# Kernel tuning notes

Measured on AMD Instinct MI355X. Metric: run time of the kernel, lower is better.

Reference implementation:

```python
import jax, jax.numpy as jnp
import numpy as np

N, K, D = 500000, 16, 16


def setup_inputs() -> dict:
    key = jax.random.key(0)
    k1, k2, k3, k4 = jax.random.split(key, 4)
    x = jax.random.normal(k1, (N, D), dtype=jnp.float32)
    # mixture weights: positive, sum to 1, shape (1, K)
    pi = jax.nn.softmax(jax.random.normal(k2, (1, K), dtype=jnp.float32), axis=-1)
    mu = jax.random.normal(k3, (K, 1, D), dtype=jnp.float32)
    # SPD covariance per cluster: A A^T / D + I
    A = jax.random.normal(k4, (K, D, D), dtype=jnp.float32)
    Sigma = jnp.einsum('kde,kfe->kdf', A, A) / D + jnp.eye(D, dtype=jnp.float32)
    return {"x": x, "pi": pi, "mu": mu, "Sigma": Sigma}


def reference(x, pi, mu, Sigma):
    # Batched MultivariateNormal log_prob over K clusters (replaces the
    # Python loop over torch.distributions.MultivariateNormal).
    d = x.shape[-1]
    L = jnp.linalg.cholesky(Sigma)                      # (K, D, D)
    diff = x[None, :, :] - mu                           # (K, N, D) via mu (K,1,D)
    # solve L y = diff^T per cluster -> Mahalanobis = ||y||^2
    y = jax.vmap(lambda Lk, dk: jax.scipy.linalg.solve_triangular(Lk, dk.T, lower=True))(L, diff)  # (K, D, N)
    maha = jnp.sum(y * y, axis=1)                       # (K, N)
    half_logdet = jnp.sum(jnp.log(jnp.diagonal(L, axis1=-2, axis2=-1)), axis=-1)  # (K,)
    log2pi = jnp.log(jnp.asarray(2.0 * np.pi, dtype=x.dtype))
    logp = -0.5 * (maha + d * log2pi) - half_logdet[:, None]  # (K, N)
    res_k = jnp.exp(logp).T * pi                        # (N, K), pi broadcasts from (1,K)
    res = res_k / jnp.sum(res_k, axis=1, keepdims=True)  # (N, K)
    return res
```

## Files before the change

kernel.cpp:

```cpp
#include <hip/hip_runtime.h>
#include <math.h>

#define D 16
#define K 16
#define BLK 256
#define PK_WORDS 96

typedef _Float16 h2 __attribute__((ext_vector_type(2)));

__host__ __device__ constexpr int tri(int i, int j) { return i * (i + 1) / 2 + j; }
__host__ __device__ constexpr int rowoff(int i) {
    int s = 0;
    for (int r = 0; r < i; ++r) s += (r + 2) / 2;
    return s;
}

static __device__ __forceinline__ float fdot2f(h2 a, h2 b, float c) {
#if __has_builtin(__builtin_amdgcn_fdot2)
    return __builtin_amdgcn_fdot2(a, b, c, false);
#else
    return fmaf((float)a.x, (float)b.x, fmaf((float)a.y, (float)b.y, c));
#endif
}

static __device__ __forceinline__ unsigned pack2(float f0, float f1) {
    _Float16 h0 = (_Float16)f0, h1 = (_Float16)f1;
    unsigned short b0 = __builtin_bit_cast(unsigned short, h0);
    unsigned short b1 = __builtin_bit_cast(unsigned short, h1);
    return ((unsigned)b1 << 16) | (unsigned)b0;
}

__global__ __launch_bounds__(64) void gmm_prep(
    const float* __restrict__ pi, const float* __restrict__ mu,
    const float* __restrict__ Sigma, float* __restrict__ P)
{
    const int k = threadIdx.x;
    if (k >= K) return;

    float M[tri(D - 1, D - 1) + 1];

#pragma unroll
    for (int i = 0; i < D; ++i)
#pragma unroll
        for (int j = 0; j <= i; ++j)
            M[tri(i, j)] = Sigma[k * D * D + i * D + j];

    float hl = 0.f;
#pragma unroll
    for (int j = 0; j < D; ++j) {
        float s = M[tri(j, j)];
#pragma unroll
        for (int p = 0; p < j; ++p) s -= M[tri(j, p)] * M[tri(j, p)];
        float ljj = sqrtf(s);
        M[tri(j, j)] = ljj;
        hl += logf(ljj);
        float inv = 1.f / ljj;
#pragma unroll
        for (int i = j + 1; i < D; ++i) {
            float t = M[tri(i, j)];
#pragma unroll
            for (int p = 0; p < j; ++p) t -= M[tri(i, p)] * M[tri(j, p)];
            M[tri(i, j)] = t * inv;
        }
    }

#pragma unroll
    for (int j = 0; j < D; ++j) {
        float ujj = 1.f / M[tri(j, j)];
        M[tri(j, j)] = ujj;
#pragma unroll
        for (int i = j + 1; i < D; ++i) {
            float s = 0.f;
#pragma unroll
            for (int p = j; p < i; ++p) s += M[tri(i, p)] * M[tri(p, j)];
            M[tri(i, j)] = -s / M[tri(i, i)];
        }
    }

    const float invs2 = 0.70710678118654752440f;
    float* Pk = P + k * PK_WORDS;
    unsigned* Pu = (unsigned*)Pk;

    Pk[0] = logf(pi[k]) - hl;
#pragma unroll
    for (int i = 0; i < D; ++i) {
        float acc = 0.f;
#pragma unroll
        for (int j = 0; j <= i; ++j) acc += M[tri(i, j)] * mu[k * D + j];
        Pk[1 + i] = -(acc * invs2);
    }
#pragma unroll
    for (int i = 0; i < D; ++i) {
        const int np = (i + 2) / 2;
#pragma unroll
        for (int p = 0; p < np; ++p) {
            float f0 = M[tri(i, 2 * p)] * invs2;
            float f1 = (2 * p + 1 <= i) ? M[tri(i, 2 * p + 1)] * invs2 : 0.f;
            Pu[17 + rowoff(i) + p] = pack2(f0, f1);
        }
    }
#pragma unroll
    for (int q = 89; q < PK_WORDS; ++q) Pu[q] = 0;
}

__global__ __launch_bounds__(BLK) void gmm_main(
    const float* __restrict__ x, const float* __restrict__ P,
    float* __restrict__ out, int N)
{
    const int tid = threadIdx.x;
    const long long n = (long long)blockIdx.x * BLK + tid;
    const bool ok = n < (long long)N;

    float4 xr0 = {0, 0, 0, 0}, xr1 = xr0, xr2 = xr0, xr3 = xr0;
    if (ok) {
        const float4* p = (const float4*)(x + n * D);
        xr0 = p[0]; xr1 = p[1]; xr2 = p[2]; xr3 = p[3];
    }

    h2 xp[8];
    xp[0] = (h2){(_Float16)xr0.x, (_Float16)xr0.y};
    xp[1] = (h2){(_Float16)xr0.z, (_Float16)xr0.w};
    xp[2] = (h2){(_Float16)xr1.x, (_Float16)xr1.y};
    xp[3] = (h2){(_Float16)xr1.z, (_Float16)xr1.w};
    xp[4] = (h2){(_Float16)xr2.x, (_Float16)xr2.y};
    xp[5] = (h2){(_Float16)xr2.z, (_Float16)xr2.w};
    xp[6] = (h2){(_Float16)xr3.x, (_Float16)xr3.y};
    xp[7] = (h2){(_Float16)xr3.z, (_Float16)xr3.w};

    float r[K];
#pragma unroll
    for (int k = 0; k < K; ++k) {
        const float* __restrict__ Pk = P + k * PK_WORDS;
        const unsigned* __restrict__ Uk = (const unsigned*)(Pk + 17);
        float acc = 0.f;
#pragma unroll
        for (int i = 0; i < D; ++i) {
            float y = Pk[1 + i];
            const int np = (i + 2) / 2;
#pragma unroll
            for (int p = 0; p < np; ++p) {
                h2 u = __builtin_bit_cast(h2, Uk[rowoff(i) + p]);
                y = fdot2f(u, xp[p], y);
            }
            acc = fmaf(y, y, acc);
        }
        r[k] = Pk[0] - acc;
    }

    float mx = r[0];
#pragma unroll
    for (int k = 1; k < K; ++k) mx = fmaxf(mx, r[k]);
    float sum = 0.f;
#pragma unroll
    for (int k = 0; k < K; ++k) {
        float e = __expf(r[k] - mx);
        r[k] = e;
        sum += e;
    }
    float inv = 1.f / sum;
    if (ok) {
        float4* po = (float4*)(out + n * D);
        po[0] = (float4){r[0] * inv,  r[1] * inv,  r[2] * inv,  r[3] * inv};
        po[1] = (float4){r[4] * inv,  r[5] * inv,  r[6] * inv,  r[7] * inv};
        po[2] = (float4){r[8] * inv,  r[9] * inv,  r[10] * inv, r[11] * inv};
        po[3] = (float4){r[12] * inv, r[13] * inv, r[14] * inv, r[15] * inv};
    }
}

extern "C" void kernel_launch(void* const* d_in, const int* in_sizes, int n_in,
                              void* d_out, int out_size, void* d_ws, size_t ws_size,
                              hipStream_t stream) {
    const float* x     = (const float*)d_in[0];
    const float* pi    = (const float*)d_in[1];
    const float* mu    = (const float*)d_in[2];
    const float* Sigma = (const float*)d_in[3];
    float* out = (float*)d_out;
    const int N = in_sizes[0] / D;

    float* P = (float*)d_ws;

    gmm_prep<<<1, 64, 0, stream>>>(pi, mu, Sigma, P);

    const int grid = (N + BLK - 1) / BLK;
    gmm_main<<<grid, BLK, 0, stream>>>(x, P, out, N);
}
```

Before: 118.6 us.

## Map clusters to lanes with register-resident factors and persistent prefetching grid

Each lane now handles one cluster for one of four points per wavefront, keeping that cluster's packed inverse-Cholesky factors and offsets in registers instead of reloading all sixteen clusters' parameters per point. The softmax over clusters becomes a 16-lane shuffle reduction. A fixed 1024-block grid-stride loop prefetches the next point's row while computing the current one. Each lane redundantly loads the full 64-byte x row, and outputs become scalar stores, which may cost bandwidth efficiency.

```diff
diff --git a/kernel.cpp b/kernel.cpp
--- a/kernel.cpp
+++ b/kernel.cpp
@@ -4,6 +4,7 @@
 #define D 16
 #define K 16
 #define BLK 256
+#define GRID 1024
 #define PK_WORDS 96
 
 typedef _Float16 h2 __attribute__((ext_vector_type(2)));
@@ -103,67 +104,92 @@
     for (int q = 89; q < PK_WORDS; ++q) Pu[q] = 0;
 }
 
-__global__ __launch_bounds__(BLK) void gmm_main(
+__global__ __launch_bounds__(BLK, 3) void gmm_main(
     const float* __restrict__ x, const float* __restrict__ P,
     float* __restrict__ out, int N)
 {
-    const int tid = threadIdx.x;
-    const long long n = (long long)blockIdx.x * BLK + tid;
-    const bool ok = n < (long long)N;
-
-    float4 xr0 = {0, 0, 0, 0}, xr1 = xr0, xr2 = xr0, xr3 = xr0;
-    if (ok) {
+    const int tid  = threadIdx.x;
+    const int lane = tid & 63;
+    const int k    = lane & 15;
+    const int q    = lane >> 4;
+
+    const long long wid = (long long)blockIdx.x * (BLK / 64) + (tid >> 6);
+    const long long nw  = (long long)gridDim.x * (BLK / 64);
+    const long long G   = ((long long)N + 3) >> 2;
+
+    const float* __restrict__ Pk = P + k * PK_WORDS;
+    const unsigned* __restrict__ Uk = (const unsigned*)(Pk + 17);
+    const float ck = Pk[0];
+    float nt[D];
+#pragma unroll
+    for (int i = 0; i < D; ++i) nt[i] = Pk[1 + i];
+    unsigned Ur[72];
+#pragma unroll
+    for (int p = 0; p < 72; ++p) Ur[p] = Uk[p];
+
+    if (wid >= G) return;
+
+    long long g = wid;
+    float4 xa0, xa1, xa2, xa3;
+    {
+        long long n = g * 4 + q;
+        if (n >= N) n = N - 1;
         const float4* p = (const float4*)(x + n * D);
-        xr0 = p[0]; xr1 = p[1]; xr2 = p[2]; xr3 = p[3];
-    }
-
-    h2 xp[8];
-    xp[0] = (h2){(_Float16)xr0.x, (_Float16)xr0.y};
-    xp[1] = (h2){(_Float16)xr0.z, (_Float16)xr0.w};
-    xp[2] = (h2){(_Float16)xr1.x, (_Float16)xr1.y};
-    xp[3] = (h2){(_Float16)xr1.z, (_Float16)xr1.w};
-    xp[4] = (h2){(_Float16)xr2.x, (_Float16)xr2.y};
-    xp[5] = (h2){(_Float16)xr2.z, (_Float16)xr2.w};
-    xp[6] = (h2){(_Float16)xr3.x, (_Float16)xr3.y};
-    xp[7] = (h2){(_Float16)xr3.z, (_Float16)xr3.w};
-
-    float r[K];
-#pragma unroll
-    for (int k = 0; k < K; ++k) {
-        const float* __restrict__ Pk = P + k * PK_WORDS;
-        const unsigned* __restrict__ Uk = (const unsigned*)(Pk + 17);
+        xa0 = p[0]; xa1 = p[1]; xa2 = p[2]; xa3 = p[3];
+    }
+
+    while (true) {
+        const long long g_next = g + nw;
+
+        float4 xb0, xb1, xb2, xb3;
+        {
+            long long n = g_next * 4 + q;
+            if (g_next >= G || n >= N) n = 0;
+            const float4* p = (const float4*)(x + n * D);
+            xb0 = p[0]; xb1 = p[1]; xb2 = p[2]; xb3 = p[3];
+        }
+
+        h2 xp[8];
+        xp[0] = (h2){(_Float16)xa0.x, (_Float16)xa0.y};
+        xp[1] = (h2){(_Float16)xa0.z, (_Float16)xa0.w};
+        xp[2] = (h2){(_Float16)xa1.x, (_Float16)xa1.y};
+        xp[3] = (h2){(_Float16)xa1.z, (_Float16)xa1.w};
+        xp[4] = (h2){(_Float16)xa2.x, (_Float16)xa2.y};
+        xp[5] = (h2){(_Float16)xa2.z, (_Float16)xa2.w};
+        xp[6] = (h2){(_Float16)xa3.x, (_Float16)xa3.y};
+        xp[7] = (h2){(_Float16)xa3.z, (_Float16)xa3.w};
+
         float acc = 0.f;
 #pragma unroll
         for (int i = 0; i < D; ++i) {
-            float y = Pk[1 + i];
+            float y = nt[i];
             const int np = (i + 2) / 2;
 #pragma unroll
-            for (int p = 0; p < np; ++p) {
-                h2 u = __builtin_bit_cast(h2, Uk[rowoff(i) + p]);
-                y = fdot2f(u, xp[p], y);
-            }
+            for (int p = 0; p < np; ++p)
+                y = fdot2f(__builtin_bit_cast(h2, Ur[rowoff(i) + p]), xp[p], y);
             acc = fmaf(y, y, acc);
         }
-        r[k] = Pk[0] - acc;
-    }
-
-    float mx = r[0];
-#pragma unroll
-    for (int k = 1; k < K; ++k) mx = fmaxf(mx, r[k]);
-    float sum = 0.f;
-#pragma unroll
-    for (int k = 0; k < K; ++k) {
-        float e = __expf(r[k] - mx);
-        r[k] = e;
-        sum += e;
-    }
-    float inv = 1.f / sum;
-    if (ok) {
-        float4* po = (float4*)(out + n * D);
-        po[0] = (float4){r[0] * inv,  r[1] * inv,  r[2] * inv,  r[3] * inv};
-        po[1] = (float4){r[4] * inv,  r[5] * inv,  r[6] * inv,  r[7] * inv};
-        po[2] = (float4){r[8] * inv,  r[9] * inv,  r[10] * inv, r[11] * inv};
-        po[3] = (float4){r[12] * inv, r[13] * inv, r[14] * inv, r[15] * inv};
+        const float logit = ck - acc;
+
+        float m = logit;
+        m = fmaxf(m, __shfl_xor(m, 1));
+        m = fmaxf(m, __shfl_xor(m, 2));
+        m = fmaxf(m, __shfl_xor(m, 4));
+        m = fmaxf(m, __shfl_xor(m, 8));
+        const float e = __expf(logit - m);
+        float s = e;
+        s += __shfl_xor(s, 1);
+        s += __shfl_xor(s, 2);
+        s += __shfl_xor(s, 4);
+        s += __shfl_xor(s, 8);
+
+        const long long n = g * 4 + q;
+        if (n < (long long)N)
+            out[n * K + k] = e / s;
+
+        if (g_next >= G) break;
+        g = g_next;
+        xa0 = xb0; xa1 = xb1; xa2 = xb2; xa3 = xb3;
     }
 }
 
@@ -181,6 +207,5 @@
 
     gmm_prep<<<1, 64, 0, stream>>>(pi, mu, Sigma, P);
 
-    const int grid = (N + BLK - 1) / BLK;
-    gmm_main<<<grid, BLK, 0, stream>>>(x, P, out, N);
-}
+    gmm_main<<<GRID, BLK, 0, stream>>>(x, P, out, N);
+}
```

After: 139.5 us. +17.6%, slower.

## Recast Mahalanobis as quadratic-feature matmul on MFMA with persistent grid

Applied to the files above, without the earlier changes.

Expands each cluster's quadratic form into weights over pairwise products x_i*x_j plus linear and constant terms, precomputed in the prep kernel. The main kernel builds fp16 product features per row and evaluates all 16 clusters with 16x16x32 f16 MFMA instructions. The softmax over clusters is done with cross-lane shuffles. A fixed persistent grid with next-tile prefetch of x replaces one thread per row. The aim is to move the triangular-solve dot products onto matrix cores, at the cost of fp16 rounding on products of x, which may hurt accuracy for large |x|.

```diff
diff --git a/kernel.cpp b/kernel.cpp
--- a/kernel.cpp
+++ b/kernel.cpp
@@ -4,41 +4,32 @@
 #define D 16
 #define K 16
 #define BLK 256
-#define PK_WORDS 96
-
-typedef _Float16 h2 __attribute__((ext_vector_type(2)));
+#define GRID 1024
+#define NFEAT 160
+
+typedef __fp16 f16x8 __attribute__((ext_vector_type(8)));
+typedef float  f32x4 __attribute__((ext_vector_type(4)));
 
 __host__ __device__ constexpr int tri(int i, int j) { return i * (i + 1) / 2 + j; }
-__host__ __device__ constexpr int rowoff(int i) {
-    int s = 0;
-    for (int r = 0; r < i; ++r) s += (r + 2) / 2;
-    return s;
-}
-
-static __device__ __forceinline__ float fdot2f(h2 a, h2 b, float c) {
-#if __has_builtin(__builtin_amdgcn_fdot2)
-    return __builtin_amdgcn_fdot2(a, b, c, false);
-#else
-    return fmaf((float)a.x, (float)b.x, fmaf((float)a.y, (float)b.y, c));
-#endif
-}
-
-static __device__ __forceinline__ unsigned pack2(float f0, float f1) {
-    _Float16 h0 = (_Float16)f0, h1 = (_Float16)f1;
-    unsigned short b0 = __builtin_bit_cast(unsigned short, h0);
-    unsigned short b1 = __builtin_bit_cast(unsigned short, h1);
-    return ((unsigned)b1 << 16) | (unsigned)b0;
+
+static __device__ __forceinline__ unsigned short f16b(float f) {
+    _Float16 h = (_Float16)f;
+    return __builtin_bit_cast(unsigned short, h);
+}
+static __device__ __forceinline__ unsigned pkrtz(float a, float b) {
+    auto t = __builtin_amdgcn_cvt_pkrtz(a, b);
+    return __builtin_bit_cast(unsigned, t);
 }
 
 __global__ __launch_bounds__(64) void gmm_prep(
     const float* __restrict__ pi, const float* __restrict__ mu,
-    const float* __restrict__ Sigma, float* __restrict__ P)
+    const float* __restrict__ Sigma, unsigned short* __restrict__ W,
+    float* __restrict__ cvals)
 {
     const int k = threadIdx.x;
     if (k >= K) return;
 
-    float M[tri(D - 1, D - 1) + 1];
-
+    float M[136];
 #pragma unroll
     for (int i = 0; i < D; ++i)
 #pragma unroll
@@ -63,7 +54,6 @@
             M[tri(i, j)] = t * inv;
         }
     }
-
 #pragma unroll
     for (int j = 0; j < D; ++j) {
         float ujj = 1.f / M[tri(j, j)];
@@ -76,94 +66,138 @@
             M[tri(i, j)] = -s / M[tri(i, i)];
         }
     }
-
     const float invs2 = 0.70710678118654752440f;
-    float* Pk = P + k * PK_WORDS;
-    unsigned* Pu = (unsigned*)Pk;
-
-    Pk[0] = logf(pi[k]) - hl;
+#pragma unroll
+    for (int t = 0; t < 136; ++t) M[t] *= invs2;
+
+    float tv[D];
+    float gamma = 0.f;
 #pragma unroll
     for (int i = 0; i < D; ++i) {
-        float acc = 0.f;
-#pragma unroll
-        for (int j = 0; j <= i; ++j) acc += M[tri(i, j)] * mu[k * D + j];
-        Pk[1 + i] = -(acc * invs2);
-    }
-#pragma unroll
-    for (int i = 0; i < D; ++i) {
-        const int np = (i + 2) / 2;
-#pragma unroll
-        for (int p = 0; p < np; ++p) {
-            float f0 = M[tri(i, 2 * p)] * invs2;
-            float f1 = (2 * p + 1 <= i) ? M[tri(i, 2 * p + 1)] * invs2 : 0.f;
-            Pu[17 + rowoff(i) + p] = pack2(f0, f1);
-        }
-    }
-#pragma unroll
-    for (int q = 89; q < PK_WORDS; ++q) Pu[q] = 0;
-}
-
-__global__ __launch_bounds__(BLK) void gmm_main(
-    const float* __restrict__ x, const float* __restrict__ P,
-    float* __restrict__ out, int N)
+        float a = 0.f;
+#pragma unroll
+        for (int j = 0; j <= i; ++j) a += M[tri(i, j)] * mu[k * D + j];
+        tv[i] = a;
+        gamma += a * a;
+    }
+    cvals[k] = logf(pi[k]) - hl - gamma;
+
+    unsigned short* Wk = W + k * NFEAT;
+#pragma unroll
+    for (int d = 0; d <= 8; ++d)
+#pragma unroll
+        for (int i = 0; i < D; ++i) {
+            const int b = (i + d) & 15;
+            const int lo = (i < b) ? i : b;
+            const int hi = (i < b) ? b : i;
+            float s = 0.f;
+#pragma unroll
+            for (int t = hi; t < D; ++t) s += M[tri(t, lo)] * M[tri(t, hi)];
+            const float w = (d == 0) ? -s : ((d == 8) ? -s : -2.f * s);
+            Wk[16 * d + i] = f16b(w);
+        }
+#pragma unroll
+    for (int m = 0; m < D; ++m) {
+        float s = 0.f;
+#pragma unroll
+        for (int t = m; t < D; ++t) s += tv[t] * M[tri(t, m)];
+        Wk[144 + m] = f16b(2.f * s);
+    }
+}
+
+__global__ __launch_bounds__(BLK, 4) void gmm_main(
+    const float* __restrict__ x, const unsigned short* __restrict__ W,
+    const float* __restrict__ cvals, float* __restrict__ out, int N)
 {
-    const int tid = threadIdx.x;
-    const long long n = (long long)blockIdx.x * BLK + tid;
-    const bool ok = n < (long long)N;
-
-    float4 xr0 = {0, 0, 0, 0}, xr1 = xr0, xr2 = xr0, xr3 = xr0;
-    if (ok) {
-        const float4* p = (const float4*)(x + n * D);
-        xr0 = p[0]; xr1 = p[1]; xr2 = p[2]; xr3 = p[3];
-    }
-
-    h2 xp[8];
-    xp[0] = (h2){(_Float16)xr0.x, (_Float16)xr0.y};
-    xp[1] = (h2){(_Float16)xr0.z, (_Float16)xr0.w};
-    xp[2] = (h2){(_Float16)xr1.x, (_Float16)xr1.y};
-    xp[3] = (h2){(_Float16)xr1.z, (_Float16)xr1.w};
-    xp[4] = (h2){(_Float16)xr2.x, (_Float16)xr2.y};
-    xp[5] = (h2){(_Float16)xr2.z, (_Float16)xr2.w};
-    xp[6] = (h2){(_Float16)xr3.x, (_Float16)xr3.y};
-    xp[7] = (h2){(_Float16)xr3.z, (_Float16)xr3.w};
-
-    float r[K];
-#pragma unroll
-    for (int k = 0; k < K; ++k) {
-        const float* __restrict__ Pk = P + k * PK_WORDS;
-        const unsigned* __restrict__ Uk = (const unsigned*)(Pk + 17);
-        float acc = 0.f;
-#pragma unroll
-        for (int i = 0; i < D; ++i) {
-            float y = Pk[1 + i];
-            const int np = (i + 2) / 2;
-#pragma unroll
-            for (int p = 0; p < np; ++p) {
-                h2 u = __builtin_bit_cast(h2, Uk[rowoff(i) + p]);
-                y = fdot2f(u, xp[p], y);
+    const int tid  = threadIdx.x;
+    const int lane = tid & 63;
+    const int col  = lane & 15;
+    const int quad = lane >> 4;
+    const bool qhi = (quad & 2) != 0;
+    const int i0   = (quad & 1) * 8;
+
+    f16x8 Af[5];
+#pragma unroll
+    for (int s = 0; s < 5; ++s) {
+        const uint4* p = (const uint4*)(W + col * NFEAT + s * 32 + quad * 8);
+        uint4 v = *p;
+        Af[s] = __builtin_bit_cast(f16x8, v);
+    }
+    const f32x4 cv = *(const f32x4*)(cvals + quad * 4);
+
+    const long long T  = ((long long)N + 15) >> 4;
+    long long tile     = (long long)blockIdx.x * (BLK / 64) + (tid >> 6);
+    const long long nw = (long long)GRID * (BLK / 64);
+    if (tile >= T) return;
+
+    float4 xa0, xa1, xa2, xa3;
+    {
+        long long n = tile * 16 + col;
+        if (n >= N) n = N - 1;
+        const float* row = x + n * D;
+        xa0 = *(const float4*)(row + i0);
+        xa1 = *(const float4*)(row + i0 + 4);
+        xa2 = *(const float4*)(row + (i0 ^ 8));
+        xa3 = *(const float4*)(row + (i0 ^ 8) + 4);
+    }
+
+    while (true) {
+        const long long tnext = tile + nw;
+        float4 xb0, xb1, xb2, xb3;
+        {
+            long long n2 = tnext * 16 + col;
+            if (tnext >= T || n2 >= (long long)N) n2 = 0;
+            const float* row = x + n2 * D;
+            xb0 = *(const float4*)(row + i0);
+            xb1 = *(const float4*)(row + i0 + 4);
+            xb2 = *(const float4*)(row + (i0 ^ 8));
+            xb3 = *(const float4*)(row + (i0 ^ 8) + 4);
+        }
+
+        const float xr[16] = {xa0.x, xa0.y, xa0.z, xa0.w,
+                              xa1.x, xa1.y, xa1.z, xa1.w,
+                              xa2.x, xa2.y, xa2.z, xa2.w,
+                              xa3.x, xa3.y, xa3.z, xa3.w};
+
+        f32x4 acc = {0.f, 0.f, 0.f, 0.f};
+#pragma unroll
+        for (int s = 0; s < 5; ++s) {
+            float pr[8];
+#pragma unroll
+            for (int j = 0; j < 8; ++j) {
+                float xbv;
+                if (s < 4)
+                    xbv = qhi ? xr[(j + 2 * s + 1) & 15] : xr[(j + 2 * s) & 15];
+                else
+                    xbv = qhi ? 1.0f : xr[(j + 8) & 15];
+                pr[j] = xr[j] * xbv;
             }
-            acc = fmaf(y, y, acc);
-        }
-        r[k] = Pk[0] - acc;
-    }
-
-    float mx = r[0];
-#pragma unroll
-    for (int k = 1; k < K; ++k) mx = fmaxf(mx, r[k]);
-    float sum = 0.f;
-#pragma unroll
-    for (int k = 0; k < K; ++k) {
-        float e = __expf(r[k] - mx);
-        r[k] = e;
-        sum += e;
-    }
-    float inv = 1.f / sum;
-    if (ok) {
-        float4* po = (float4*)(out + n * D);
-        po[0] = (float4){r[0] * inv,  r[1] * inv,  r[2] * inv,  r[3] * inv};
-        po[1] = (float4){r[4] * inv,  r[5] * inv,  r[6] * inv,  r[7] * inv};
-        po[2] = (float4){r[8] * inv,  r[9] * inv,  r[10] * inv, r[11] * inv};
-        po[3] = (float4){r[12] * inv, r[13] * inv, r[14] * inv, r[15] * inv};
+            uint4 bw = {pkrtz(pr[0], pr[1]), pkrtz(pr[2], pr[3]),
+                        pkrtz(pr[4], pr[5]), pkrtz(pr[6], pr[7])};
+            f16x8 Bf = __builtin_bit_cast(f16x8, bw);
+            acc = __builtin_amdgcn_mfma_f32_16x16x32_f16(Af[s], Bf, acc, 0, 0, 0);
+        }
+
+        f32x4 l = acc + cv;
+        float mx = fmaxf(fmaxf(l.x, l.y), fmaxf(l.z, l.w));
+        mx = fmaxf(mx, __shfl_xor(mx, 16));
+        mx = fmaxf(mx, __shfl_xor(mx, 32));
+        float e0 = __expf(l.x - mx), e1 = __expf(l.y - mx);
+        float e2 = __expf(l.z - mx), e3 = __expf(l.w - mx);
+        float ss = e0 + e1 + e2 + e3;
+        ss += __shfl_xor(ss, 16);
+        ss += __shfl_xor(ss, 32);
+        const float inv = 1.f / ss;
+
+        const long long n = tile * 16 + col;
+        if (n < (long long)N) {
+            float4* po = (float4*)(out + n * K + quad * 4);
+            *po = (float4){e0 * inv, e1 * inv, e2 * inv, e3 * inv};
+        }
+
+        if (tnext >= T) break;
+        tile = tnext;
+        xa0 = xb0; xa1 = xb1; xa2 = xb2; xa3 = xb3;
     }
 }
 
@@ -177,10 +211,9 @@
     float* out = (float*)d_out;
     const int N = in_sizes[0] / D;
 
-    float* P = (float*)d_ws;
-
-    gmm_prep<<<1, 64, 0, stream>>>(pi, mu, Sigma, P);
-
-    const int grid = (N + BLK - 1) / BLK;
-    gmm_main<<<grid, BLK, 0, stream>>>(x, P, out, N);
-}
+    unsigned short* W = (unsigned short*)d_ws;
+    float* cvals = (float*)((char*)d_ws + K * NFEAT * sizeof(unsigned short));
+
+    gmm_prep<<<1, 64, 0, stream>>>(pi, mu, Sigma, W, cvals);
+    gmm_main<<<GRID, BLK, 0, stream>>>(x, W, cvals, out, N);
+}
```

Result: slower. 131.1 us (+10.5%).
